# Optimization experiments

Measured on AMD Instinct MI355X. Metric: run time of the kernel, lower is better.

## Reference

```python
import jax, jax.numpy as jnp
import numpy as np

N = 100000
E = 1600000
IN_C = 128
HID = 32
HEADS = 4
NUM_CLASSES = 16
NEG_SLOPE = 0.2


def setup_inputs() -> dict:
    key = jax.random.key(0)
    ks = jax.random.split(key, 10)
    x = jax.random.normal(ks[0], (N, IN_C), dtype=jnp.float32)
    edge_index = jax.random.randint(ks[1], (2, E), 0, N, dtype=jnp.int32)
    s1 = 1.0 / np.sqrt(IN_C)
    s2 = 1.0 / np.sqrt(HID * HEADS)
    W1 = jax.random.normal(ks[2], (IN_C, HEADS * HID), dtype=jnp.float32) * s1
    att_src1 = jax.random.normal(ks[3], (HEADS, HID), dtype=jnp.float32) * s1
    att_dst1 = jax.random.normal(ks[4], (HEADS, HID), dtype=jnp.float32) * s1
    b1 = jnp.zeros((HEADS * HID,), dtype=jnp.float32)
    W2 = jax.random.normal(ks[5], (HEADS * HID, NUM_CLASSES), dtype=jnp.float32) * s2
    att_src2 = jax.random.normal(ks[6], (1, NUM_CLASSES), dtype=jnp.float32) * s2
    att_dst2 = jax.random.normal(ks[7], (1, NUM_CLASSES), dtype=jnp.float32) * s2
    b2 = jnp.zeros((NUM_CLASSES,), dtype=jnp.float32)
    return {"x": x, "edge_index": edge_index,
            "W1": W1, "att_src1": att_src1, "att_dst1": att_dst1, "b1": b1,
            "W2": W2, "att_src2": att_src2, "att_dst2": att_dst2, "b2": b2}


def _gat_conv(x, src, dst, W, att_src, att_dst, b):
    # PyG GATConv: shared linear for src/dst, additive attention, segment softmax over dst.
    n = x.shape[0]
    H, C = att_src.shape
    h = (x @ W).reshape(n, H, C)                       # [N, H, C]
    a_s = jnp.einsum('nhc,hc->nh', h, att_src)          # [N, H]
    a_d = jnp.einsum('nhc,hc->nh', h, att_dst)          # [N, H]
    e = a_s[src] + a_d[dst]                             # [E, H]
    e = jnp.where(e >= 0, e, NEG_SLOPE * e)             # leaky_relu(0.2)
    # numerically stable segment softmax over destination node groups
    e_max = jax.ops.segment_max(e, dst, num_segments=n)
    e_exp = jnp.exp(e - e_max[dst])
    denom = jax.ops.segment_sum(e_exp, dst, num_segments=n)
    alpha = e_exp / denom[dst]                          # [E, H]
    msg = h[src] * alpha[:, :, None]                    # [E, H, C]
    out = jax.ops.segment_sum(msg, dst, num_segments=n) # [N, H, C]
    return out.reshape(n, H * C) + b


def reference(x, edge_index, W1, att_src1, att_dst1, b1, W2, att_src2, att_dst2, b2):
    n = x.shape[0]
    # add_self_loops=True (PyG default), same augmented edge set for both layers
    loop = jnp.arange(n, dtype=edge_index.dtype)
    src = jnp.concatenate([edge_index[0], loop])
    dst = jnp.concatenate([edge_index[1], loop])
    h = _gat_conv(x, src, dst, W1, att_src1, att_dst1, b1)
    h = jax.nn.elu(h)
    out = _gat_conv(h, src, dst, W2, att_src2, att_dst2, b2)
    return out
```

## Files before the change

kernel.cpp:

```cpp
#include <hip/hip_runtime.h>
#include <hip/hip_bf16.h>
#include <math.h>


typedef unsigned short u16;
typedef unsigned int u32;
typedef __attribute__((ext_vector_type(8))) short bf16x8;
typedef __attribute__((ext_vector_type(4))) float f32x4;

__device__ __forceinline__ float eluf(float v) { return v > 0.f ? v : expm1f(v); }
__device__ __forceinline__ u16 f2bf(float f) {
    u32 u = __float_as_uint(f);
    u += 0x7fff + ((u >> 16) & 1);
    return (u16)(u >> 16);
}
__device__ __forceinline__ float bf2f(u16 u) {
    return __uint_as_float(((u32)u) << 16);
}
__device__ __forceinline__ float expleaky(float e) {
    float m = e >= 0.f ? 1.44269504f : 0.28853901f;
    return exp2f(e * m);
}

__global__ __launch_bounds__(256) void ksetup(
    const float* __restrict__ W1, const float* __restrict__ W2,
    const float* __restrict__ ats2, const float* __restrict__ atd2,
    u16* __restrict__ w1fh, u16* __restrict__ w1fl,
    float* __restrict__ u, float* __restrict__ v, u16* __restrict__ w2tb,
    int* __restrict__ deg, int N)
{
    const int b = blockIdx.x, tid = threadIdx.x;
    if (b < 64) {
        int idx = b * 256 + tid;
        int j = idx & 7, l = (idx >> 3) & 63, q = (idx >> 9) & 3, ct = idx >> 11;
        int k = q * 32 + (l >> 4) * 8 + j;
        int n = ct * 16 + (l & 15);
        float w = W1[k * 128 + n];
        u16 hv = f2bf(w);
        w1fh[idx] = hv;
        w1fl[idx] = f2bf(w - bf2f(hv));
    } else if (b == 64) {
        if (tid < 128) {
            float su = 0.f, sv = 0.f;
            #pragma unroll
            for (int j = 0; j < 16; ++j) {
                float w = W2[tid * 16 + j];
                su = fmaf(w, ats2[j], su);
                sv = fmaf(w, atd2[j], sv);
                w2tb[j * 128 + tid] = f2bf(w);
            }
            u[tid] = su; v[tid] = sv;
        }
    } else {
        int z = (b - 65) * 1024 + tid * 4;
        if (z < N) *(int4*)&deg[z] = make_int4(0, 0, 0, 0);
    }
}

__global__ __launch_bounds__(256) void mega1(
    const float* __restrict__ x, const u16* __restrict__ w1fh,
    const u16* __restrict__ w1fl,
    const float* __restrict__ att_s, const float* __restrict__ att_d,
    u16* __restrict__ h1b, float* __restrict__ as1, float* __restrict__ ad1,
    int N,
    const int* __restrict__ ei, int* __restrict__ deg, int* __restrict__ rank,
    int E, int Bh1)
{
    __shared__ u16 lh[8192];
    __shared__ u16 ll[8192];
    if (blockIdx.x >= Bh1) {
        int e = (blockIdx.x - Bh1) * 256 + threadIdx.x;
        if (e < E) rank[e] = atomicAdd(&deg[ei[E + e]], 1);
        return;
    }
    const int tid = threadIdx.x;
    const int wv = tid >> 6, lane = tid & 63;
    const int base = blockIdx.x * 64 + wv * 16;
    const int m = lane & 15, quad = lane >> 4;

    int arow = base + m;
    if (arow >= N) arow = 0;
    const float* xr = &x[(size_t)arow * 128 + quad * 8];
    bf16x8 ah[4], al[4];
    #pragma unroll
    for (int q = 0; q < 4; ++q) {
        float4 f0 = *(const float4*)&xr[q * 32];
        float4 f1 = *(const float4*)&xr[q * 32 + 4];
        float fv[8] = {f0.x, f0.y, f0.z, f0.w, f1.x, f1.y, f1.z, f1.w};
        union { u16 us[8]; bf16x8 v; } hh, lu;
        #pragma unroll
        for (int j = 0; j < 8; ++j) {
            u16 h = f2bf(fv[j]);
            hh.us[j] = h;
            lu.us[j] = f2bf(fv[j] - bf2f(h));
        }
        ah[q] = hh.v; al[q] = lu.v;
    }

    for (int p = 0; p < 2; ++p) {
        __syncthreads();
        #pragma unroll
        for (int i = 0; i < 4; ++i) {
            int fi = (tid + i * 256) * 8;
            *(uint4*)&lh[fi] = *(const uint4*)&w1fh[p * 8192 + fi];
            *(uint4*)&ll[fi] = *(const uint4*)&w1fl[p * 8192 + fi];
        }
        __syncthreads();
        #pragma unroll
        for (int hh2 = 0; hh2 < 2; ++hh2) {
            const int h = p * 2 + hh2;
            float sp[4] = {0.f, 0.f, 0.f, 0.f};
            float dp[4] = {0.f, 0.f, 0.f, 0.f};
            #pragma unroll
            for (int sub = 0; sub < 2; ++sub) {
                const int ctl = hh2 * 2 + sub;
                const int ct = p * 4 + ctl;
                f32x4 acc = {0.f, 0.f, 0.f, 0.f};
                #pragma unroll
                for (int q = 0; q < 4; ++q) {
                    const int off = ((ctl * 4 + q) * 64 + lane) * 8;
                    bf16x8 bh = *(const bf16x8*)&lh[off];
                    bf16x8 bl = *(const bf16x8*)&ll[off];
                    acc = __builtin_amdgcn_mfma_f32_16x16x32_bf16(ah[q], bh, acc, 0, 0, 0);
                    acc = __builtin_amdgcn_mfma_f32_16x16x32_bf16(al[q], bh, acc, 0, 0, 0);
                    acc = __builtin_amdgcn_mfma_f32_16x16x32_bf16(ah[q], bl, acc, 0, 0, 0);
                }
                const float cs = att_s[h * 32 + sub * 16 + m];
                const float cd = att_d[h * 32 + sub * 16 + m];
                #pragma unroll
                for (int r = 0; r < 4; ++r) {
                    int rr = base + quad * 4 + r;
                    if (rr < N) h1b[(size_t)rr * 128 + ct * 16 + m] = f2bf(acc[r]);
                    sp[r] = fmaf(acc[r], cs, sp[r]);
                    dp[r] = fmaf(acc[r], cd, dp[r]);
                }
            }
            #pragma unroll
            for (int r = 0; r < 4; ++r) {
                sp[r] += __shfl_xor(sp[r], 1); sp[r] += __shfl_xor(sp[r], 2);
                sp[r] += __shfl_xor(sp[r], 4); sp[r] += __shfl_xor(sp[r], 8);
                dp[r] += __shfl_xor(dp[r], 1); dp[r] += __shfl_xor(dp[r], 2);
                dp[r] += __shfl_xor(dp[r], 4); dp[r] += __shfl_xor(dp[r], 8);
            }
            if (m == 0) {
                #pragma unroll
                for (int r = 0; r < 4; ++r) {
                    int rr = base + quad * 4 + r;
                    if (rr < N) {
                        as1[rr * 4 + h] = sp[r];
                        ad1[rr * 4 + h] = dp[r];
                    }
                }
            }
        }
    }
}

__global__ __launch_bounds__(256) void kscan1(
    const int* __restrict__ deg, int* __restrict__ rowptr,
    int* __restrict__ bsum, int N)
{
    __shared__ int lds[256];
    const int t = threadIdx.x;
    const int base = blockIdx.x * 1024 + t * 4;
    int v[4];
    int s = 0;
    #pragma unroll
    for (int j = 0; j < 4; ++j) {
        v[j] = (base + j < N) ? deg[base + j] : 0;
        s += v[j];
    }
    lds[t] = s;
    __syncthreads();
    for (int off = 1; off < 256; off <<= 1) {
        int y = (t >= off) ? lds[t - off] : 0;
        __syncthreads();
        lds[t] += y;
        __syncthreads();
    }
    int run = lds[t] - s;
    #pragma unroll
    for (int j = 0; j < 4; ++j) {
        if (base + j < N) rowptr[base + j] = run;
        run += v[j];
    }
    if (t == 255) bsum[blockIdx.x] = lds[255];
}

__global__ __launch_bounds__(128) void kscan2(int* __restrict__ bsum, int NB)
{
    __shared__ int lds[128];
    const int t = threadIdx.x;
    int v = (t < NB) ? bsum[t] : 0;
    lds[t] = v;
    __syncthreads();
    for (int off = 1; off < 128; off <<= 1) {
        int y = (t >= off) ? lds[t - off] : 0;
        __syncthreads();
        lds[t] += y;
        __syncthreads();
    }
    if (t < NB) bsum[t] = lds[t] - v;
}

__global__ __launch_bounds__(256) void kscat(
    const int* __restrict__ ei, const int* __restrict__ rowptr,
    const int* __restrict__ bsum, const int* __restrict__ rank,
    int* __restrict__ colidx, int E)
{
    int e = blockIdx.x * 256 + threadIdx.x;
    if (e >= E) return;
    int s = ei[e], d = ei[E + e];
    colidx[rowptr[d] + bsum[d >> 10] + rank[e]] = s;
}

__global__ __launch_bounds__(256) void kg1(
    const int* __restrict__ rowptr, const int* __restrict__ bsum,
    const int* __restrict__ colidx,
    const u16* __restrict__ h1b, const float* __restrict__ as1,
    const float* __restrict__ ad1, const float* __restrict__ b1,
    const float* __restrict__ u, const float* __restrict__ v,
    u16* __restrict__ x2b, float* __restrict__ as2, float* __restrict__ ad2,
    int N, int E)
{
    const int d = blockIdx.x * 4 + (threadIdx.x >> 6);
    if (d >= N) return;
    const int lane = threadIdx.x & 63;
    const int c = lane * 2;
    const int headB = lane >> 4;
    const int headA = lane & 3;
    const int eA = lane >> 2;

    const float adA = ad1[d * 4 + headA];
    const float wself = expleaky(as1[d * 4 + headB] + ad1[d * 4 + headB]);
    u32 hd = *(const u32*)&h1b[(d << 7) + c];
    float accx = wself * bf2f((u16)hd);
    float accy = wself * bf2f((u16)(hd >> 16));
    float den = wself;

    int i0r = rowptr[d] + bsum[d >> 10];
    int i1r = (d + 1 == N) ? E : rowptr[d + 1] + bsum[(d + 1) >> 10];
    const int i0 = __builtin_amdgcn_readfirstlane(i0r);
    const int i1 = __builtin_amdgcn_readfirstlane(i1r);

    for (int i = i0; i < i1; i += 16) {
        const int nb = min(16, i1 - i);
        const int ii = i + eA;
        const int iic = ii < i1 ? ii : i0;
        int sAv = colidx[iic];
        float wA = expleaky(as1[(sAv << 2) + headA] + adA);
        wA = (ii < i1) ? wA : 0.f;
        int e = 0;
        for (; e + 8 <= nb; e += 8) {
            int s0 = colidx[i + e + 0];
            int s1 = colidx[i + e + 1];
            int s2 = colidx[i + e + 2];
            int s3 = colidx[i + e + 3];
            int s4 = colidx[i + e + 4];
            int s5 = colidx[i + e + 5];
            int s6 = colidx[i + e + 6];
            int s7 = colidx[i + e + 7];
            float w0 = __shfl(wA, ((e + 0) << 2) + headB);
            float w1 = __shfl(wA, ((e + 1) << 2) + headB);
            float w2 = __shfl(wA, ((e + 2) << 2) + headB);
            float w3 = __shfl(wA, ((e + 3) << 2) + headB);
            float w4 = __shfl(wA, ((e + 4) << 2) + headB);
            float w5 = __shfl(wA, ((e + 5) << 2) + headB);
            float w6 = __shfl(wA, ((e + 6) << 2) + headB);
            float w7 = __shfl(wA, ((e + 7) << 2) + headB);
            u32 v0 = *(const u32*)&h1b[(s0 << 7) + c];
            u32 v1 = *(const u32*)&h1b[(s1 << 7) + c];
            u32 v2 = *(const u32*)&h1b[(s2 << 7) + c];
            u32 v3 = *(const u32*)&h1b[(s3 << 7) + c];
            u32 v4 = *(const u32*)&h1b[(s4 << 7) + c];
            u32 v5 = *(const u32*)&h1b[(s5 << 7) + c];
            u32 v6 = *(const u32*)&h1b[(s6 << 7) + c];
            u32 v7 = *(const u32*)&h1b[(s7 << 7) + c];
            accx = fmaf(w0, bf2f((u16)v0), accx); accy = fmaf(w0, bf2f((u16)(v0 >> 16)), accy);
            accx = fmaf(w1, bf2f((u16)v1), accx); accy = fmaf(w1, bf2f((u16)(v1 >> 16)), accy);
            accx = fmaf(w2, bf2f((u16)v2), accx); accy = fmaf(w2, bf2f((u16)(v2 >> 16)), accy);
            accx = fmaf(w3, bf2f((u16)v3), accx); accy = fmaf(w3, bf2f((u16)(v3 >> 16)), accy);
            accx = fmaf(w4, bf2f((u16)v4), accx); accy = fmaf(w4, bf2f((u16)(v4 >> 16)), accy);
            accx = fmaf(w5, bf2f((u16)v5), accx); accy = fmaf(w5, bf2f((u16)(v5 >> 16)), accy);
            accx = fmaf(w6, bf2f((u16)v6), accx); accy = fmaf(w6, bf2f((u16)(v6 >> 16)), accy);
            accx = fmaf(w7, bf2f((u16)v7), accx); accy = fmaf(w7, bf2f((u16)(v7 >> 16)), accy);
            den += ((w0 + w1) + (w2 + w3)) + ((w4 + w5) + (w6 + w7));
        }
        for (; e < nb; ++e) {
            int s = colidx[i + e];
            float w = __shfl(wA, (e << 2) + headB);
            u32 hv = *(const u32*)&h1b[(s << 7) + c];
            accx = fmaf(w, bf2f((u16)hv), accx);
            accy = fmaf(w, bf2f((u16)(hv >> 16)), accy);
            den += w;
        }
    }

    const float inv = 1.f / den;
    const float2 bv = *(const float2*)&b1[c];
    const float x2a = eluf(fmaf(accx, inv, bv.x));
    const float x2c = eluf(fmaf(accy, inv, bv.y));

    u32 pk = ((u32)f2bf(x2c) << 16) | (u32)f2bf(x2a);
    *(u32*)&x2b[(d << 7) + c] = pk;

    const float2 uv = *(const float2*)&u[c];
    const float2 vv = *(const float2*)&v[c];
    float sA = fmaf(x2a, uv.x, x2c * uv.y);
    float sB = fmaf(x2a, vv.x, x2c * vv.y);
    #pragma unroll
    for (int m = 1; m < 64; m <<= 1) {
        sA += __shfl_xor(sA, m);
        sB += __shfl_xor(sB, m);
    }
    if (lane == 0) { as2[d] = sA; ad2[d] = sB; }
}

__global__ __launch_bounds__(256) void kh2(
    const u16* __restrict__ x2b, const u16* __restrict__ w2tb,
    u16* __restrict__ h2b, int N)
{
    const int wv = threadIdx.x >> 6, lane = threadIdx.x & 63;
    const int n0 = blockIdx.x * 64 + wv * 16;
    if (n0 >= N) return;
    const int m = lane & 15;
    const int kq = lane >> 4;
    bf16x8 bfr[4];
    #pragma unroll
    for (int q = 0; q < 4; ++q)
        bfr[q] = *(const bf16x8*)&w2tb[m * 128 + q * 32 + kq * 8];

    int ar = n0 + m;
    if (ar >= N) ar = N - 1;
    const u16* arow = &x2b[((size_t)ar << 7) + kq * 8];
    f32x4 acc = {0.f, 0.f, 0.f, 0.f};
    #pragma unroll
    for (int q = 0; q < 4; ++q) {
        bf16x8 af = *(const bf16x8*)&arow[q * 32];
        acc = __builtin_amdgcn_mfma_f32_16x16x32_bf16(af, bfr[q], acc, 0, 0, 0);
    }
    #pragma unroll
    for (int r = 0; r < 4; ++r) {
        int rr = n0 + kq * 4 + r;
        if (rr < N) h2b[((size_t)rr << 4) + m] = f2bf(acc[r]);
    }
}

__global__ __launch_bounds__(256) void kg2(
    const int* __restrict__ rowptr, const int* __restrict__ bsum,
    const int* __restrict__ colidx,
    const u16* __restrict__ h2b, const float* __restrict__ as2,
    const float* __restrict__ ad2, const float* __restrict__ b2,
    float* __restrict__ out, int N, int E)
{
    const int d = blockIdx.x * 4 + (threadIdx.x >> 6);
    if (d >= N) return;
    const int lane = threadIdx.x & 63;
    const int ch = lane & 7, g = lane >> 3;

    const float ad_d = ad2[d];
    float acc0 = 0.f, acc1 = 0.f, den = 0.f;
    int i0r = rowptr[d] + bsum[d >> 10];
    int i1r = (d + 1 == N) ? E : rowptr[d + 1] + bsum[(d + 1) >> 10];
    const int i0 = __builtin_amdgcn_readfirstlane(i0r);
    const int i1 = __builtin_amdgcn_readfirstlane(i1r);

    for (int i = i0; i < i1; i += 64) {
        const int nb = min(64, i1 - i);
        const int idx = i + lane;
        const int idxc = idx < i1 ? idx : i0;
        int sA = colidx[idxc];
        float wA = expleaky(as2[sA] + ad_d);
        wA = (idx < i1) ? wA : 0.f;
        const int kU = (nb + 7) >> 3;
        for (int k = 0; k < kU; ++k) {
            int e = g + 8 * k;
            int ec = e < nb ? e : 0;
            float w = __shfl(wA, ec);
            int s = __shfl(sA, ec);
            if (e >= nb) w = 0.f;
            u32 hv = *(const u32*)&h2b[(s << 4) + ch * 2];
            acc0 = fmaf(w, bf2f((u16)hv), acc0);
            acc1 = fmaf(w, bf2f((u16)(hv >> 16)), acc1);
            den += w;
        }
    }
    acc0 += __shfl_xor(acc0, 8); acc0 += __shfl_xor(acc0, 16); acc0 += __shfl_xor(acc0, 32);
    acc1 += __shfl_xor(acc1, 8); acc1 += __shfl_xor(acc1, 16); acc1 += __shfl_xor(acc1, 32);
    den  += __shfl_xor(den, 8);  den  += __shfl_xor(den, 16);  den  += __shfl_xor(den, 32);

    const float wself = expleaky(as2[d] + ad_d);
    u32 hd = *(const u32*)&h2b[(d << 4) + ch * 2];
    acc0 = fmaf(wself, bf2f((u16)hd), acc0);
    acc1 = fmaf(wself, bf2f((u16)(hd >> 16)), acc1);
    den += wself;
    if (g == 0) {
        float2 ov = {acc0 / den + b2[ch * 2], acc1 / den + b2[ch * 2 + 1]};
        *(float2*)&out[(d << 4) + ch * 2] = ov;
    }
}

extern "C" void kernel_launch(void* const* d_in, const int* in_sizes, int n_in,
                              void* d_out, int out_size, void* d_ws, size_t ws_size,
                              hipStream_t stream) {
    const float* x    = (const float*)d_in[0];
    const int*   ei   = (const int*)d_in[1];
    const float* W1   = (const float*)d_in[2];
    const float* ats1 = (const float*)d_in[3];
    const float* atd1 = (const float*)d_in[4];
    const float* b1   = (const float*)d_in[5];
    const float* W2   = (const float*)d_in[6];
    const float* ats2 = (const float*)d_in[7];
    const float* atd2 = (const float*)d_in[8];
    const float* b2   = (const float*)d_in[9];
    float* out = (float*)d_out;
    const int N = in_sizes[0] / 128;
    const int E = in_sizes[1] / 2;

    u16* h1b   = (u16*)d_ws;
    u16* x2b   = h1b + (size_t)N * 128;
    u16* h2b   = x2b + (size_t)N * 128;
    u16* w2tb  = h2b + (size_t)N * 16;
    u16* w1fh  = w2tb + 2048;
    u16* w1fl  = w1fh + 16384;
    float* as1 = (float*)(w1fl + 16384);
    float* ad1 = as1 + (size_t)N * 4;
    float* as2 = ad1 + (size_t)N * 4;
    float* ad2 = as2 + N;
    float* u   = ad2 + N;
    float* v   = u + 128;
    int* deg    = (int*)(v + 128);
    int* rowptr = deg + ((N + 7) & ~3);
    int* bsum   = rowptr + ((N + 7) & ~3);
    int* colidx = bsum + 128;
    int* rank   = colidx + E;

    const int NB  = (N + 1023) / 1024;
    const int Bh1 = (N + 63) / 64;
    const int Bhist = (E + 255) / 256;

    hipLaunchKernelGGL(ksetup, dim3(65 + NB), dim3(256), 0, stream,
                       W1, W2, ats2, atd2, w1fh, w1fl, u, v, w2tb, deg, N);
    hipLaunchKernelGGL(mega1, dim3(Bh1 + Bhist), dim3(256), 0, stream,
                       x, w1fh, w1fl, ats1, atd1, h1b, as1, ad1, N,
                       ei, deg, rank, E, Bh1);
    hipLaunchKernelGGL(kscan1, dim3(NB), dim3(256), 0, stream,
                       deg, rowptr, bsum, N);
    hipLaunchKernelGGL(kscan2, dim3(1), dim3(128), 0, stream, bsum, NB);
    hipLaunchKernelGGL(kscat, dim3((E + 255) / 256), dim3(256), 0, stream,
                       ei, rowptr, bsum, rank, colidx, E);
    hipLaunchKernelGGL(kg1, dim3((N + 3) / 4), dim3(256), 0, stream,
                       rowptr, bsum, colidx, h1b, as1, ad1, b1, u, v,
                       x2b, as2, ad2, N, E);
    hipLaunchKernelGGL(kh2, dim3((N + 63) / 64), dim3(256), 0, stream,
                       x2b, w2tb, h2b, N);
    hipLaunchKernelGGL(kg2, dim3((N + 3) / 4), dim3(256), 0, stream,
                       rowptr, bsum, colidx, h2b, as2, ad2, b2, out, N, E);
}
```

Baseline: 358.9 us.

## Merge degree histogram into GEMM blocks and coalesce h1 stores via LDS

The separate edge-histogram blocks are removed, and each GEMM block now handles a grid-strided share of the degree atomics before doing its matmul tile. The h1 accumulators are kept in registers across both weight passes. They are then staged through a padded LDS buffer that reuses the weight shared memory, so rows are written as 16-byte coalesced stores instead of scattered 2-byte stores. The attention dot products are computed afterward from the saved accumulators. This raises register use and puts the atomic work on the GEMM blocks' critical path, in exchange for fewer blocks and better store coalescing.

Result: faster. 340.5 us (-5.1%).

```diff
diff --git a/kernel.cpp b/kernel.cpp
--- a/kernel.cpp
+++ b/kernel.cpp
@@ -57,6 +57,7 @@
     }
 }
 
+#define REPSTRIDE 136
 __global__ __launch_bounds__(256) void mega1(
     const float* __restrict__ x, const u16* __restrict__ w1fh,
     const u16* __restrict__ w1fl,
@@ -64,16 +65,19 @@
     u16* __restrict__ h1b, float* __restrict__ as1, float* __restrict__ ad1,
     int N,
     const int* __restrict__ ei, int* __restrict__ deg, int* __restrict__ rank,
-    int E, int Bh1)
-{
-    __shared__ u16 lh[8192];
-    __shared__ u16 ll[8192];
-    if (blockIdx.x >= Bh1) {
-        int e = (blockIdx.x - Bh1) * 256 + threadIdx.x;
-        if (e < E) rank[e] = atomicAdd(&deg[ei[E + e]], 1);
-        return;
-    }
+    int E, int grid)
+{
+    __shared__ union {
+        struct { u16 lh[8192]; u16 ll[8192]; } w;
+        u16 rep[16384];
+    } sm;
     const int tid = threadIdx.x;
+
+    for (int e = blockIdx.x * 256 + tid; e < E; e += grid * 256) {
+        int dd = ei[E + e];
+        rank[e] = atomicAdd(&deg[dd], 1);
+    }
+
     const int wv = tid >> 6, lane = tid & 63;
     const int base = blockIdx.x * 64 + wv * 16;
     const int m = lane & 15, quad = lane >> 4;
@@ -97,62 +101,79 @@
         ah[q] = hh.v; al[q] = lu.v;
     }
 
+    f32x4 accs[8];
     for (int p = 0; p < 2; ++p) {
         __syncthreads();
         #pragma unroll
         for (int i = 0; i < 4; ++i) {
             int fi = (tid + i * 256) * 8;
-            *(uint4*)&lh[fi] = *(const uint4*)&w1fh[p * 8192 + fi];
-            *(uint4*)&ll[fi] = *(const uint4*)&w1fl[p * 8192 + fi];
-        }
-        __syncthreads();
-        #pragma unroll
-        for (int hh2 = 0; hh2 < 2; ++hh2) {
-            const int h = p * 2 + hh2;
-            float sp[4] = {0.f, 0.f, 0.f, 0.f};
-            float dp[4] = {0.f, 0.f, 0.f, 0.f};
+            *(uint4*)&sm.w.lh[fi] = *(const uint4*)&w1fh[p * 8192 + fi];
+            *(uint4*)&sm.w.ll[fi] = *(const uint4*)&w1fl[p * 8192 + fi];
+        }
+        __syncthreads();
+        #pragma unroll
+        for (int ctl = 0; ctl < 4; ++ctl) {
+            f32x4 acc = {0.f, 0.f, 0.f, 0.f};
             #pragma unroll
-            for (int sub = 0; sub < 2; ++sub) {
-                const int ctl = hh2 * 2 + sub;
-                const int ct = p * 4 + ctl;
-                f32x4 acc = {0.f, 0.f, 0.f, 0.f};
-                #pragma unroll
-                for (int q = 0; q < 4; ++q) {
-                    const int off = ((ctl * 4 + q) * 64 + lane) * 8;
-                    bf16x8 bh = *(const bf16x8*)&lh[off];
-                    bf16x8 bl = *(const bf16x8*)&ll[off];
-                    acc = __builtin_amdgcn_mfma_f32_16x16x32_bf16(ah[q], bh, acc, 0, 0, 0);
-                    acc = __builtin_amdgcn_mfma_f32_16x16x32_bf16(al[q], bh, acc, 0, 0, 0);
-                    acc = __builtin_amdgcn_mfma_f32_16x16x32_bf16(ah[q], bl, acc, 0, 0, 0);
-                }
-                const float cs = att_s[h * 32 + sub * 16 + m];
-                const float cd = att_d[h * 32 + sub * 16 + m];
-                #pragma unroll
-                for (int r = 0; r < 4; ++r) {
-                    int rr = base + quad * 4 + r;
-                    if (rr < N) h1b[(size_t)rr * 128 + ct * 16 + m] = f2bf(acc[r]);
-                    sp[r] = fmaf(acc[r], cs, sp[r]);
-                    dp[r] = fmaf(acc[r], cd, dp[r]);
+            for (int q = 0; q < 4; ++q) {
+                const int off = ((ctl * 4 + q) * 64 + lane) * 8;
+                bf16x8 bh = *(const bf16x8*)&sm.w.lh[off];
+                bf16x8 bl = *(const bf16x8*)&sm.w.ll[off];
+                acc = __builtin_amdgcn_mfma_f32_16x16x32_bf16(ah[q], bh, acc, 0, 0, 0);
+                acc = __builtin_amdgcn_mfma_f32_16x16x32_bf16(al[q], bh, acc, 0, 0, 0);
+                acc = __builtin_amdgcn_mfma_f32_16x16x32_bf16(ah[q], bl, acc, 0, 0, 0);
+            }
+            accs[p * 4 + ctl] = acc;
+        }
+    }
+
+    #pragma unroll
+    for (int h = 0; h < 4; ++h) {
+        const float cs0 = att_s[h * 32 + m];
+        const float cs1 = att_s[h * 32 + 16 + m];
+        const float cd0 = att_d[h * 32 + m];
+        const float cd1 = att_d[h * 32 + 16 + m];
+        float sp[4], dp[4];
+        #pragma unroll
+        for (int r = 0; r < 4; ++r) {
+            sp[r] = fmaf(accs[2 * h][r], cs0, accs[2 * h + 1][r] * cs1);
+            dp[r] = fmaf(accs[2 * h][r], cd0, accs[2 * h + 1][r] * cd1);
+        }
+        #pragma unroll
+        for (int r = 0; r < 4; ++r) {
+            sp[r] += __shfl_xor(sp[r], 1); sp[r] += __shfl_xor(sp[r], 2);
+            sp[r] += __shfl_xor(sp[r], 4); sp[r] += __shfl_xor(sp[r], 8);
+            dp[r] += __shfl_xor(dp[r], 1); dp[r] += __shfl_xor(dp[r], 2);
+            dp[r] += __shfl_xor(dp[r], 4); dp[r] += __shfl_xor(dp[r], 8);
+        }
+        if (m == 0) {
+            #pragma unroll
+            for (int r = 0; r < 4; ++r) {
+                int rr = base + quad * 4 + r;
+                if (rr < N) {
+                    as1[rr * 4 + h] = sp[r];
+                    ad1[rr * 4 + h] = dp[r];
                 }
             }
-            #pragma unroll
-            for (int r = 0; r < 4; ++r) {
-                sp[r] += __shfl_xor(sp[r], 1); sp[r] += __shfl_xor(sp[r], 2);
-                sp[r] += __shfl_xor(sp[r], 4); sp[r] += __shfl_xor(sp[r], 8);
-                dp[r] += __shfl_xor(dp[r], 1); dp[r] += __shfl_xor(dp[r], 2);
-                dp[r] += __shfl_xor(dp[r], 4); dp[r] += __shfl_xor(dp[r], 8);
-            }
-            if (m == 0) {
-                #pragma unroll
-                for (int r = 0; r < 4; ++r) {
-                    int rr = base + quad * 4 + r;
-                    if (rr < N) {
-                        as1[rr * 4 + h] = sp[r];
-                        ad1[rr * 4 + h] = dp[r];
-                    }
-                }
-            }
-        }
+        }
+    }
+
+    __syncthreads();
+    u16* rep = sm.rep + wv * (16 * REPSTRIDE);
+    #pragma unroll
+    for (int ct = 0; ct < 8; ++ct) {
+        #pragma unroll
+        for (int r = 0; r < 4; ++r)
+            rep[(quad * 4 + r) * REPSTRIDE + ct * 16 + m] = f2bf(accs[ct][r]);
+    }
+    const int rr0 = lane >> 2, cc = lane & 3;
+    #pragma unroll
+    for (int round = 0; round < 4; ++round) {
+        int chunk = cc + 4 * round;
+        uint4 vv = *(const uint4*)&rep[rr0 * REPSTRIDE + chunk * 8];
+        int grow = base + rr0;
+        if (grow < N)
+            *(uint4*)&h1b[(size_t)grow * 128 + chunk * 8] = vv;
     }
 }
 
@@ -437,11 +458,10 @@
 
     const int NB  = (N + 1023) / 1024;
     const int Bh1 = (N + 63) / 64;
-    const int Bhist = (E + 255) / 256;
 
     hipLaunchKernelGGL(ksetup, dim3(65 + NB), dim3(256), 0, stream,
                        W1, W2, ats2, atd2, w1fh, w1fl, u, v, w2tb, deg, N);
-    hipLaunchKernelGGL(mega1, dim3(Bh1 + Bhist), dim3(256), 0, stream,
+    hipLaunchKernelGGL(mega1, dim3(Bh1), dim3(256), 0, stream,
                        x, w1fh, w1fl, ats1, atd1, h1b, as1, ad1, N,
                        ei, deg, rank, E, Bh1);
     hipLaunchKernelGGL(kscan1, dim3(NB), dim3(256), 0, stream,
```
